# Performance work log

Measured on AMD Instinct MI355X. Metric: run time of the kernel, lower is better.

The kernel has to match this reference:

```python
import jax, jax.numpy as jnp
import numpy as np

K = 1024  # number of sampled points (self.k)


def _fps_single(pts):
    """Furthest point sampling for one cloud. pts: [N, 3] -> idx: [K] int32.
    Matches pointnet2 FPS: start at index 0, iteratively pick the point
    farthest (max of min-squared-distance) from the selected set."""
    N = pts.shape[0]

    def step(carry, _):
        dists, cur = carry
        d = jnp.sum((pts - pts[cur]) ** 2, axis=-1)  # [N]
        dists = jnp.minimum(dists, d)
        nxt = jnp.argmax(dists).astype(jnp.int32)
        return (dists, nxt), cur

    init = (jnp.full((N,), jnp.inf, dtype=pts.dtype), jnp.int32(0))
    _, idx = jax.lax.scan(step, init, None, length=K)
    return idx  # [K]


def setup_inputs() -> dict:
    key = jax.random.key(0)
    k1, k2 = jax.random.split(key)
    B, N, C = 8, 32768, 128
    xyz = jax.random.normal(k1, (B, 3, N), dtype=jnp.float32)
    feature = jax.random.normal(k2, (B, C, N), dtype=jnp.float32)
    return {"xyz": xyz, "feature": feature}


def reference(xyz, feature):
    # xyz: [B, 3, N], feature: [B, C, N]
    pts = jnp.transpose(xyz, (0, 2, 1))            # [B, N, 3]
    idx = jax.vmap(_fps_single)(pts)                # [B, K] int32
    # gather along the point axis (axis=2)
    node_static = jnp.take_along_axis(xyz, idx[:, None, :], axis=2)      # [B, 3, K]
    node_feature = jnp.take_along_axis(feature, idx[:, None, :], axis=2)  # [B, C, K]
    return (node_static, node_feature)
```

## Files before the change

### kernel.cpp

```cpp
#include <hip/hip_runtime.h>


#define BATCH 8
#define NPTS 32768
#define KSEL 1024
#define CFEAT 128
#define WPB 8
#define LOCN (NPTS / WPB)
#define TPB 1024
#define NWAVE (TPB / 64)

typedef unsigned long long u64;

#define AT_ST(p, v) __hip_atomic_store((p), (v), __ATOMIC_RELAXED, __HIP_MEMORY_SCOPE_AGENT)
#define AT_LD(p)    __hip_atomic_load((p), __ATOMIC_RELAXED, __HIP_MEMORY_SCOPE_AGENT)

__global__ void
__attribute__((amdgpu_flat_work_group_size(TPB, TPB)))
fps_kernel(const float* __restrict__ xyz, char* __restrict__ ws) {
    int* idxbuf = (int*)ws;
    u64* slots  = (u64*)(ws + 32768);

    __shared__ float swd[NWAVE];
    __shared__ int   swn[NWAVE];
    __shared__ int   sgw;

    const int bid  = blockIdx.x;
    const int b    = bid & 7;
    const int blk  = bid >> 3;
    const int tid  = threadIdx.x;
    const int lane = tid & 63;
    const int wid  = tid >> 6;

    const float* Xp = xyz + (size_t)b * 3 * NPTS;
    const float* Yp = Xp + NPTS;
    const float* Zp = Xp + 2 * NPTS;

    const int o4 = blk * (LOCN / 4) + tid;
    const float4 x4 = ((const float4*)Xp)[o4];
    const float4 y4 = ((const float4*)Yp)[o4];
    const float4 z4 = ((const float4*)Zp)[o4];
    const float* xe = (const float*)&x4;
    const float* ye = (const float*)&y4;
    const float* ze = (const float*)&z4;
    float ds[4] = {__builtin_inff(), __builtin_inff(),
                   __builtin_inff(), __builtin_inff()};

    if (blk == 0 && tid == 0) idxbuf[(size_t)b * KSEL] = 0;
    float cx = Xp[0], cy = Yp[0], cz = Zp[0];

    for (int t = 1; t < KSEL; ++t) {
        float bd = -__builtin_inff();
        int   be = 0;
#pragma unroll
        for (int e = 0; e < 4; ++e) {
            const float dx = xe[e] - cx;
            const float dy = ye[e] - cy;
            const float dz = ze[e] - cz;
            const float d = __fadd_rn(__fadd_rn(__fmul_rn(dx, dx), __fmul_rn(dy, dy)),
                                      __fmul_rn(dz, dz));
            const float nd = fminf(ds[e], d);
            ds[e] = nd;
            const bool gt = nd > bd;
            bd = gt ? nd : bd;
            be = gt ? e : be;
        }
        int bn = tid * 4 + be;
#pragma unroll
        for (int off = 32; off >= 1; off >>= 1) {
            const float od = __shfl_xor(bd, off);
            const int   on = __shfl_xor(bn, off);
            if (od > bd || (od == bd && on < bn)) { bd = od; bn = on; }
        }
        if (lane == 0) { swd[wid] = bd; swn[wid] = bn; }
        __syncthreads();

        if (wid == 0) {
            float rd = swd[lane & 15];
            int   rn = swn[lane & 15];
#pragma unroll
            for (int off = 8; off >= 1; off >>= 1) {
                const float od = __shfl_xor(rd, off);
                const int   on = __shfl_xor(rn, off);
                if (od > rd || (od == rd && on < rn)) { rd = od; rn = on; }
            }
            u64* slotbase = &slots[(size_t)(t & 1) * (BATCH * WPB) + b * WPB];
            if (lane == 0) {
                const int gn = blk * LOCN + rn;
                const u64 v = ((u64)__float_as_uint(rd) << 32)
                            | ((u64)(t & 1023) << 15) | (u64)gn;
                AT_ST(&slotbase[blk], v);
            }
            u64 v;
            do { v = AT_LD(&slotbase[lane & 7]); }
            while (!__all((int)((v >> 15) & 1023) == t));
            float od = __uint_as_float((unsigned)(v >> 32));
            int   on = (int)(v & 32767);
#pragma unroll
            for (int off = 4; off >= 1; off >>= 1) {
                const float pd = __shfl_xor(od, off);
                const int   pn = __shfl_xor(on, off);
                if (pd > od || (pd == od && pn < on)) { od = pd; on = pn; }
            }
            if (lane == 0) sgw = on;
        }
        __syncthreads();
        const int gw = sgw;
        if (blk == 0 && tid == 0) idxbuf[(size_t)b * KSEL + t] = gw;
        cx = Xp[gw]; cy = Yp[gw]; cz = Zp[gw];
    }
}

__global__ void gather_kernel(const float* __restrict__ xyz,
                              const float* __restrict__ feat,
                              const int* __restrict__ idxbuf,
                              float* __restrict__ out) {
    const int SN = BATCH * 3 * KSEL;
    const int total = SN + BATCH * CFEAT * KSEL;
    const int i = blockIdx.x * blockDim.x + threadIdx.x;
    if (i >= total) return;
    if (i < SN) {
        const int b = i / (3 * KSEL);
        const int r = i - b * 3 * KSEL;
        const int c = r / KSEL;
        const int k = r - c * KSEL;
        const int n = idxbuf[b * KSEL + k];
        out[i] = xyz[((size_t)b * 3 + c) * NPTS + n];
    } else {
        const int i2 = i - SN;
        const int b = i2 / (CFEAT * KSEL);
        const int r = i2 - b * CFEAT * KSEL;
        const int c = r / KSEL;
        const int k = r - c * KSEL;
        const int n = idxbuf[b * KSEL + k];
        out[SN + i2] = feat[((size_t)b * CFEAT + c) * NPTS + n];
    }
}

extern "C" void kernel_launch(void* const* d_in, const int* in_sizes, int n_in,
                              void* d_out, int out_size, void* d_ws, size_t ws_size,
                              hipStream_t stream) {
    const float* xyz  = (const float*)d_in[0];
    const float* feat = (const float*)d_in[1];
    float* out = (float*)d_out;
    char* ws = (char*)d_ws;

    hipMemsetAsync(ws + 32768, 0, 2 * BATCH * WPB * sizeof(u64), stream);

    void* args[] = {(void*)&xyz, (void*)&ws};
    hipLaunchCooperativeKernel((const void*)fps_kernel,
                               dim3(BATCH * WPB), dim3(TPB), args, 0, stream);

    int* idxbuf = (int*)d_ws;
    const int total = BATCH * 3 * KSEL + BATCH * CFEAT * KSEL;
    gather_kernel<<<(total + 255) / 256, 256, 0, stream>>>(xyz, feat, idxbuf, out);
}
```

Before: 2.529 ms.

## Halve FPS block size with eight points per thread and batch spin-wait polls

Each FPS block now has 512 threads instead of 1024, and every thread holds eight points in registers instead of four. This makes the per-iteration block reduction shorter, with 8 waves instead of 16 feeding the shared-memory stage, which cuts the latency of each of the serial selection steps. The cross-block spin-wait now issues four atomic loads back to back before checking them, so poll latency overlaps. The costs are more serial distance work per thread and more register use.

```diff
diff --git a/kernel.cpp b/kernel.cpp
--- a/kernel.cpp
+++ b/kernel.cpp
@@ -7,13 +7,15 @@
 #define CFEAT 128
 #define WPB 8
 #define LOCN (NPTS / WPB)
-#define TPB 1024
+#define TPB 512
+#define PPT 8
 #define NWAVE (TPB / 64)
 
 typedef unsigned long long u64;
 
 #define AT_ST(p, v) __hip_atomic_store((p), (v), __ATOMIC_RELAXED, __HIP_MEMORY_SCOPE_AGENT)
 #define AT_LD(p)    __hip_atomic_load((p), __ATOMIC_RELAXED, __HIP_MEMORY_SCOPE_AGENT)
+#define TAG(v)      ((int)(((v) >> 15) & 1023))
 
 __global__ void
 __attribute__((amdgpu_flat_work_group_size(TPB, TPB)))
@@ -35,16 +37,20 @@
     const float* Xp = xyz + (size_t)b * 3 * NPTS;
     const float* Yp = Xp + NPTS;
     const float* Zp = Xp + 2 * NPTS;
+    const float4* X4 = (const float4*)Xp;
+    const float4* Y4 = (const float4*)Yp;
+    const float4* Z4 = (const float4*)Zp;
 
-    const int o4 = blk * (LOCN / 4) + tid;
-    const float4 x4 = ((const float4*)Xp)[o4];
-    const float4 y4 = ((const float4*)Yp)[o4];
-    const float4 z4 = ((const float4*)Zp)[o4];
-    const float* xe = (const float*)&x4;
-    const float* ye = (const float*)&y4;
-    const float* ze = (const float*)&z4;
-    float ds[4] = {__builtin_inff(), __builtin_inff(),
-                   __builtin_inff(), __builtin_inff()};
+    const int f4 = blk * (LOCN / 4) + 2 * tid;
+    const float4 xa = X4[f4], xb = X4[f4 + 1];
+    const float4 ya = Y4[f4], yb = Y4[f4 + 1];
+    const float4 za = Z4[f4], zb = Z4[f4 + 1];
+    float xs[PPT] = {xa.x, xa.y, xa.z, xa.w, xb.x, xb.y, xb.z, xb.w};
+    float ys[PPT] = {ya.x, ya.y, ya.z, ya.w, yb.x, yb.y, yb.z, yb.w};
+    float zs[PPT] = {za.x, za.y, za.z, za.w, zb.x, zb.y, zb.z, zb.w};
+    float ds[PPT];
+#pragma unroll
+    for (int e = 0; e < PPT; ++e) ds[e] = __builtin_inff();
 
     if (blk == 0 && tid == 0) idxbuf[(size_t)b * KSEL] = 0;
     float cx = Xp[0], cy = Yp[0], cz = Zp[0];
@@ -53,10 +59,10 @@
         float bd = -__builtin_inff();
         int   be = 0;
 #pragma unroll
-        for (int e = 0; e < 4; ++e) {
-            const float dx = xe[e] - cx;
-            const float dy = ye[e] - cy;
-            const float dz = ze[e] - cz;
+        for (int e = 0; e < PPT; ++e) {
+            const float dx = xs[e] - cx;
+            const float dy = ys[e] - cy;
+            const float dz = zs[e] - cz;
             const float d = __fadd_rn(__fadd_rn(__fmul_rn(dx, dx), __fmul_rn(dy, dy)),
                                       __fmul_rn(dz, dz));
             const float nd = fminf(ds[e], d);
@@ -65,7 +71,7 @@
             bd = gt ? nd : bd;
             be = gt ? e : be;
         }
-        int bn = tid * 4 + be;
+        int bn = tid * PPT + be;
 #pragma unroll
         for (int off = 32; off >= 1; off >>= 1) {
             const float od = __shfl_xor(bd, off);
@@ -76,10 +82,10 @@
         __syncthreads();
 
         if (wid == 0) {
-            float rd = swd[lane & 15];
-            int   rn = swn[lane & 15];
+            float rd = swd[lane & 7];
+            int   rn = swn[lane & 7];
 #pragma unroll
-            for (int off = 8; off >= 1; off >>= 1) {
+            for (int off = 4; off >= 1; off >>= 1) {
                 const float od = __shfl_xor(rd, off);
                 const int   on = __shfl_xor(rn, off);
                 if (od > rd || (od == rd && on < rn)) { rd = od; rn = on; }
@@ -91,9 +97,18 @@
                             | ((u64)(t & 1023) << 15) | (u64)gn;
                 AT_ST(&slotbase[blk], v);
             }
+            u64* sp = &slotbase[lane & 7];
             u64 v;
-            do { v = AT_LD(&slotbase[lane & 7]); }
-            while (!__all((int)((v >> 15) & 1023) == t));
+            for (;;) {
+                const u64 v0 = AT_LD(sp);
+                const u64 v1 = AT_LD(sp);
+                const u64 v2 = AT_LD(sp);
+                const u64 v3 = AT_LD(sp);
+                if (__all(TAG(v0) == t)) { v = v0; break; }
+                if (__all(TAG(v1) == t)) { v = v1; break; }
+                if (__all(TAG(v2) == t)) { v = v2; break; }
+                if (__all(TAG(v3) == t)) { v = v3; break; }
+            }
             float od = __uint_as_float((unsigned)(v >> 32));
             int   on = (int)(v & 32767);
 #pragma unroll
```

Measured after the change: 2.402 ms (median of 2 runs). -5.1%, faster.
